# Kernel tuning notes

Hardware: AMD Instinct MI355X
Metric: run time of the kernel (lower is better)

Reference implementation:

```python
import jax, jax.numpy as jnp
import numpy as np

B, N, DK, H, A = 32, 4096, 128, 128, 128  # batch, src nodes, z dim, lstm hidden, attn dim
NEG_INF = -1e9


def setup_inputs() -> dict:
    key = jax.random.key(0)
    ks = jax.random.split(key, 12)
    sc = lambda *s: 1.0 / np.sqrt(s[-1])
    return {
        "z": jax.random.normal(ks[0], (B, N, DK), jnp.float32),
        "mask": jnp.ones((B, N), jnp.float32),
        "h0": jax.random.normal(ks[1], (B, H), jnp.float32),
        "c0": jax.random.normal(ks[2], (B, H), jnp.float32),
        # generate_lstm params (input=DK context vec, hidden=H), torch gate order i,f,g,o
        "W_ih": jax.random.normal(ks[3], (4 * H, DK), jnp.float32) * sc(DK),
        "W_hh": jax.random.normal(ks[4], (4 * H, H), jnp.float32) * sc(H),
        "b_ih": jnp.zeros((4 * H,), jnp.float32),
        "b_hh": jnp.zeros((4 * H,), jnp.float32),
        # coverage-attention params (Bahdanau + coverage, See et al. 2017)
        "W_x": jax.random.normal(ks[5], (2 * H, A), jnp.float32) * sc(2 * H),
        "W_z": jax.random.normal(ks[6], (DK, A), jnp.float32) * sc(DK),
        "w_c": jax.random.normal(ks[7], (A,), jnp.float32) * 0.1,
        "b_attn": jnp.zeros((A,), jnp.float32),
        "v": jax.random.normal(ks[8], (A,), jnp.float32) * sc(A),
        "n_node": 64,
    }


def reference(z, mask, h0, c0, W_ih, W_hh, b_ih, b_hh, W_x, W_z, w_c, b_attn, v, n_node):
    z_fea = jnp.einsum("bnd,da->bna", z, W_z)  # precomputed encoder features [B,N,A]
    mask_bool = mask > 0

    def step(carry, _):
        h, c, s, coverage, closs = carry
        # LSTM cell, torch gate order (i, f, g, o)
        gates = s @ W_ih.T + b_ih + h @ W_hh.T + b_hh  # [B,4H]
        i_g, f_g, g_g, o_g = jnp.split(gates, 4, axis=-1)
        c_new = jax.nn.sigmoid(f_g) * c + jax.nn.sigmoid(i_g) * jnp.tanh(g_g)
        h_new = jax.nn.sigmoid(o_g) * jnp.tanh(c_new)
        x = jnp.concatenate([h_new, c_new], axis=-1)  # [B,2H]
        # coverage attention
        dec_fea = x @ W_x  # [B,A]
        feat = jnp.tanh(z_fea + dec_fea[:, None, :] + coverage[..., None] * w_c + b_attn)
        e = jnp.einsum("bna,a->bn", feat, v)  # [B,N]
        e = jnp.where(mask_bool, e, NEG_INF)
        attn = jax.nn.softmax(e, axis=-1)  # [B,N]
        c_t = jnp.einsum("bn,bnd->bd", attn, z)  # context [B,DK]
        closs = closs + jnp.mean(jnp.sum(jnp.minimum(attn, coverage), axis=1))
        s_new = jax.lax.stop_gradient(c_t)  # torch: s = c_t.data
        coverage_new = coverage + attn
        return (h_new, c_new, s_new, coverage_new, closs), (c_t, attn)

    init = (h0, c0, jnp.zeros((B, DK), z.dtype), jnp.zeros((B, N), z.dtype), jnp.asarray(0.0, z.dtype))
    (_, _, _, _, closs), (cts, attns) = jax.lax.scan(step, init, None, length=n_node)
    text = jnp.transpose(cts, (1, 0, 2))        # [B, n_node, DK]
    attentions = jnp.transpose(attns, (1, 0, 2))  # [B, n_node, N]
    return text, attentions, closs
```

## Files before the change

### kernel.cpp

```cpp
#include <hip/hip_runtime.h>
#include <hip/hip_bf16.h>
#include <hip/hip_fp16.h>
#include <math.h>

#define B 32
#define NN 4096
#define DK 128
#define HH 128
#define AA 128
#define NCH 32
#define CHN 128

static const size_t OFF_ZF   = 0;
static const size_t OFF_ZH   = OFF_ZF + (size_t)B*NN*AA/2;
static const size_t OFF_P    = OFF_ZH + (size_t)B*NN*DK/2;
static const size_t OFF_COV  = OFF_P + (size_t)B*NN;
static const size_t OFF_SRED = OFF_COV + (size_t)B*NN;
static const size_t OFF_PCTX = OFF_SRED + 2*B;
static const size_t OFF_PSUM = OFF_PCTX + (size_t)B*NCH*DK;
static const size_t OFF_PCL  = OFF_PSUM + (size_t)B*NCH;
static const size_t OFF_DECQ = OFF_PCL + (size_t)B*NCH;
static const size_t OFF_HST  = OFF_DECQ + (size_t)B*AA;
static const size_t OFF_CST  = OFF_HST + (size_t)B*HH;
static const size_t OFF_CLA  = OFF_CST + (size_t)B*HH;

__device__ __forceinline__ float fast_tanh(float x) {
    float e = __expf(2.f * x);
    return 1.f - 2.f / (e + 1.f);
}
__device__ __forceinline__ float fast_sig(float x) {
    return 1.f / (1.f + __expf(-x));
}

__device__ void lstm_phase(int tid, int b, const float* __restrict__ sm_s,
                           float* hst, float* cst, float* decq,
                           const float* __restrict__ W_ih, const float* __restrict__ W_hh,
                           const float* __restrict__ b_ih, const float* __restrict__ b_hh,
                           const float* __restrict__ W_x, const float* __restrict__ b_attn)
{
    __shared__ float sm_h[HH];
    __shared__ float sm_g[4 * HH];
    __shared__ float sm_x[2 * HH];
    if (tid < HH) sm_h[tid] = hst[b * HH + tid];
    __syncthreads();
    if (tid < 256) {
        int j0 = tid, j1 = tid + 256;
        float g0 = b_ih[j0] + b_hh[j0];
        float g1 = b_ih[j1] + b_hh[j1];
        const float4* wi0 = (const float4*)(W_ih + (size_t)j0 * DK);
        const float4* wh0 = (const float4*)(W_hh + (size_t)j0 * HH);
        const float4* wi1 = (const float4*)(W_ih + (size_t)j1 * DK);
        const float4* wh1 = (const float4*)(W_hh + (size_t)j1 * HH);
        #pragma unroll 8
        for (int d4 = 0; d4 < DK / 4; ++d4) {
            float4 s4 = ((const float4*)sm_s)[d4];
            float4 h4 = ((const float4*)sm_h)[d4];
            float4 a0 = wi0[d4], a1 = wi1[d4];
            float4 c0 = wh0[d4], c1 = wh1[d4];
            g0 += s4.x*a0.x + s4.y*a0.y + s4.z*a0.z + s4.w*a0.w
                + h4.x*c0.x + h4.y*c0.y + h4.z*c0.z + h4.w*c0.w;
            g1 += s4.x*a1.x + s4.y*a1.y + s4.z*a1.z + s4.w*a1.w
                + h4.x*c1.x + h4.y*c1.y + h4.z*c1.z + h4.w*c1.w;
        }
        sm_g[j0] = g0; sm_g[j1] = g1;
    }
    __syncthreads();
    if (tid < HH) {
        float ig = sm_g[tid], fg = sm_g[HH + tid];
        float gg = sm_g[2 * HH + tid], og = sm_g[3 * HH + tid];
        float cold = cst[b * HH + tid];
        float cn = fast_sig(fg) * cold + fast_sig(ig) * fast_tanh(gg);
        float hn = fast_sig(og) * fast_tanh(cn);
        cst[b * HH + tid] = cn;
        hst[b * HH + tid] = hn;
        sm_x[tid] = hn;
        sm_x[HH + tid] = cn;
    }
    __syncthreads();
    if (tid < AA) {
        float df = b_attn[tid];
        #pragma unroll 8
        for (int k4 = 0; k4 < (2 * HH) / 4; ++k4) {
            float4 xv = ((const float4*)sm_x)[k4];
            df += xv.x * W_x[(size_t)(4 * k4 + 0) * AA + tid]
                + xv.y * W_x[(size_t)(4 * k4 + 1) * AA + tid]
                + xv.z * W_x[(size_t)(4 * k4 + 2) * AA + tid]
                + xv.w * W_x[(size_t)(4 * k4 + 3) * AA + tid];
        }
        decq[b * AA + tid] = df;
    }
    __syncthreads();
}

__global__ __launch_bounds__(256) void zfea_kernel(const float* __restrict__ z,
                                                   const float* __restrict__ Wz,
                                                   __half* __restrict__ zfh,
                                                   __half* __restrict__ zh)
{
    __shared__ float sz[32 * DK];
    const int tid = threadIdx.x;
    const size_t r0 = (size_t)blockIdx.x * 32;
    const float4* zsrc = (const float4*)(z + r0 * DK);
    float4* sz4 = (float4*)sz;
    #pragma unroll
    for (int i = 0; i < 4; ++i) sz4[i * 256 + tid] = zsrc[i * 256 + tid];
    __syncthreads();

    {
        __half2* zh2o = (__half2*)zh;
        #pragma unroll
        for (int k = 0; k < (32 * DK / 2) / 256; ++k) {
            int i = k * 256 + tid;
            __half2 hz = __floats2half2_rn(sz[2 * i], sz[2 * i + 1]);
            zh2o[r0 * (DK / 2) + i] = hz;
        }
    }

    const int a4 = tid & 31;
    const int g  = tid >> 5;
    float4 acc[4];
    #pragma unroll
    for (int r = 0; r < 4; ++r) acc[r] = make_float4(0.f, 0.f, 0.f, 0.f);
    const float4* Wz4 = (const float4*)Wz;
    for (int d4 = 0; d4 < 32; ++d4) {
        float4 w0 = Wz4[(4 * d4 + 0) * 32 + a4];
        float4 w1 = Wz4[(4 * d4 + 1) * 32 + a4];
        float4 w2 = Wz4[(4 * d4 + 2) * 32 + a4];
        float4 w3 = Wz4[(4 * d4 + 3) * 32 + a4];
        #pragma unroll
        for (int r = 0; r < 4; ++r) {
            float4 zv = *(const float4*)(&sz[(g * 4 + r) * DK + 4 * d4]);
            acc[r].x += zv.x * w0.x + zv.y * w1.x + zv.z * w2.x + zv.w * w3.x;
            acc[r].y += zv.x * w0.y + zv.y * w1.y + zv.z * w2.y + zv.w * w3.y;
            acc[r].z += zv.x * w0.z + zv.y * w1.z + zv.z * w2.z + zv.w * w3.z;
            acc[r].w += zv.x * w0.w + zv.y * w1.w + zv.z * w2.w + zv.w * w3.w;
        }
    }
    #pragma unroll
    for (int r = 0; r < 4; ++r) {
        __half2 h0 = __floats2half2_rn(acc[r].x, acc[r].y);
        __half2 h1 = __floats2half2_rn(acc[r].z, acc[r].w);
        __half2* dst = (__half2*)(zfh + (r0 + g * 4 + r) * AA + 4 * a4);
        dst[0] = h0;
        dst[1] = h1;
    }
}

__global__ __launch_bounds__(256) void prologue_kernel(
    const float* __restrict__ h0, const float* __restrict__ c0,
    float* cov, float* decq, float* hst, float* cst,
    float* cla, float* out_closs,
    const float* __restrict__ W_ih, const float* __restrict__ W_hh,
    const float* __restrict__ b_ih, const float* __restrict__ b_hh,
    const float* __restrict__ W_x, const float* __restrict__ b_attn)
{
    int b = blockIdx.x;
    int tid = threadIdx.x;
    float4 zero4 = make_float4(0.f, 0.f, 0.f, 0.f);
    float4* c4 = (float4*)(cov + (size_t)b * NN);
    for (int i = tid; i < NN / 4; i += 256) c4[i] = zero4;
    if (tid == 0) {
        cla[b] = 0.f;
        if (b == 0) *out_closs = 0.f;
    }
    if (tid < HH) {
        hst[b * HH + tid] = h0[b * HH + tid];
        cst[b * HH + tid] = c0[b * HH + tid];
    }
    __shared__ float sm_s[DK];
    if (tid < DK) sm_s[tid] = 0.f;
    __syncthreads();
    lstm_phase(tid, b, sm_s, hst, cst, decq, W_ih, W_hh, b_ih, b_hh, W_x, b_attn);
}

__global__ __launch_bounds__(512, 8) void attn_kernel(
    const __half* __restrict__ zh, const float* __restrict__ mask,
    const float* __restrict__ w_c, const float* __restrict__ v,
    const __half* __restrict__ zfh, float* __restrict__ p, float* __restrict__ cov,
    const float* __restrict__ Sred, float* __restrict__ pctx,
    float* __restrict__ psum, float* __restrict__ pcl,
    const float* __restrict__ decq,
    float* __restrict__ out_attn,
    int t, int T)
{
    const int tid = threadIdx.x;
    const int b = blockIdx.x & (B - 1);
    const int chunk = blockIdx.x >> 5;
    const int n0 = chunk * CHN;
    const int prv = (t ^ 1) & 1;

    __shared__ float sm_cov[CHN];
    __shared__ float sm_mask[CHN];
    __shared__ float sm_p[CHN];
    __shared__ float sm_ctx[8][DK];
    __shared__ float sm_sump[8];
    __shared__ float sm_red[2];

    if (tid < CHN) {
        int n = n0 + tid;
        size_t bn = (size_t)b * NN + n;
        float covn = cov[bn];
        float closs_part = 0.f;
        if (t > 0) {
            float invS = 1.f / Sred[prv * B + b];
            float ap = p[bn] * invS;
            __builtin_nontemporal_store(ap, &out_attn[((size_t)b * T + (t - 1)) * NN + n]);
            closs_part = fminf(ap, covn);
            covn += ap;
            cov[bn] = covn;
        }
        sm_cov[tid] = covn;
        #pragma unroll
        for (int off = 32; off; off >>= 1) closs_part += __shfl_xor(closs_part, off, 64);
        if ((tid & 63) == 0) sm_red[tid >> 6] = closs_part;
    } else if (tid < 2 * CHN) {
        sm_mask[tid - CHN] = mask[(size_t)b * NN + n0 + (tid - CHN)];
    }
    __syncthreads();

    const int w = tid >> 6, l = tid & 63;
    const int g2 = l >> 5, lane32 = l & 31;
    const float4 q4  = *(const float4*)(decq + b * AA + 4 * lane32);
    const float4 wc4 = *(const float4*)(w_c + 4 * lane32);
    const float4 v4  = *(const float4*)(v + 4 * lane32);

    float2 raw[8];
    {
        const char* zbase = (const char*)(zfh + ((size_t)b * NN + n0) * AA) + 8 * lane32;
        const int nbase = w * 16 + g2;
        #pragma unroll
        for (int it = 0; it < 8; ++it)
            raw[it] = *(const float2*)(zbase + (size_t)(nbase + 2 * it) * (AA * 2));
    }
    float sump = 0.f;
    float el[8];
    #pragma unroll
    for (int it = 0; it < 8; ++it) {
        const int nl = w * 16 + 2 * it + g2;
        const float cvn = sm_cov[nl];
        __half2 ha = *(__half2*)&raw[it].x;
        __half2 hb = *(__half2*)&raw[it].y;
        float2 fa = __half22float2(ha);
        float2 fb = __half22float2(hb);
        float x0 = fmaf(cvn, wc4.x, fa.x + q4.x);
        float x1 = fmaf(cvn, wc4.y, fa.y + q4.y);
        float x2 = fmaf(cvn, wc4.z, fb.x + q4.z);
        float x3 = fmaf(cvn, wc4.w, fb.y + q4.w);
        el[it] = fast_tanh(x0) * v4.x + fast_tanh(x1) * v4.y
               + fast_tanh(x2) * v4.z + fast_tanh(x3) * v4.w;
    }
    #pragma unroll
    for (int off = 16; off; off >>= 1) {
        #pragma unroll
        for (int it = 0; it < 8; ++it) el[it] += __shfl_xor(el[it], off, 64);
    }
    #pragma unroll
    for (int it = 0; it < 8; ++it) {
        const int nl = w * 16 + 2 * it + g2;
        float pe = (sm_mask[nl] > 0.f) ? __expf(el[it]) : 0.f;
        if (lane32 == 0) sm_p[nl] = pe;
        sump += pe;
    }
    sump += __shfl_xor(sump, 32, 64);
    if (l == 0) sm_sump[w] = sump;
    __syncthreads();

    const uint2* zh2 = (const uint2*)(zh + ((size_t)b * NN + n0) * DK);
    float4 acc = make_float4(0.f, 0.f, 0.f, 0.f);
    #pragma unroll
    for (int it = 0; it < 8; ++it) {
        const int nl = w * 16 + 2 * it + g2;
        uint2 u = zh2[(size_t)nl * 32 + lane32];
        __half2 ha = *(__half2*)&u.x;
        __half2 hb = *(__half2*)&u.y;
        float2 fa = __half22float2(ha);
        float2 fb = __half22float2(hb);
        float pe = sm_p[nl];
        acc.x = fmaf(pe, fa.x, acc.x);
        acc.y = fmaf(pe, fa.y, acc.y);
        acc.z = fmaf(pe, fb.x, acc.z);
        acc.w = fmaf(pe, fb.y, acc.w);
    }
    acc.x += __shfl_xor(acc.x, 32, 64);
    acc.y += __shfl_xor(acc.y, 32, 64);
    acc.z += __shfl_xor(acc.z, 32, 64);
    acc.w += __shfl_xor(acc.w, 32, 64);
    if (g2 == 0) *(float4*)(&sm_ctx[w][4 * lane32]) = acc;
    __syncthreads();

    if (tid < CHN) p[(size_t)b * NN + n0 + tid] = sm_p[tid];
    if (tid < DK) {
        float r = 0.f;
        #pragma unroll
        for (int ww = 0; ww < 8; ++ww) r += sm_ctx[ww][tid];
        pctx[((size_t)b * NCH + chunk) * DK + tid] = r;
    } else if (tid == DK) {
        float s8 = 0.f;
        #pragma unroll
        for (int ww = 0; ww < 8; ++ww) s8 += sm_sump[ww];
        psum[b * NCH + chunk] = s8;
    } else if (tid == DK + 1) {
        pcl[b * NCH + chunk] = sm_red[0] + sm_red[1];
    }
}

__global__ __launch_bounds__(256) void finish_kernel(
    const float* __restrict__ pctx, const float* __restrict__ psum,
    const float* __restrict__ pcl,
    float* __restrict__ Sred, float* __restrict__ cla,
    float* __restrict__ out_text,
    float* hst, float* cst, float* decq,
    const float* __restrict__ W_ih, const float* __restrict__ W_hh,
    const float* __restrict__ b_ih, const float* __restrict__ b_hh,
    const float* __restrict__ W_x, const float* __restrict__ b_attn,
    int t, int T)
{
    const int b = blockIdx.x;
    const int tid = threadIdx.x;
    const int cur = t & 1;
    __shared__ float sm_s[DK];
    __shared__ float sm_S;

    float r = 0.f;
    if (tid < DK) {
        #pragma unroll
        for (int k = 0; k < NCH; ++k)
            r += pctx[((size_t)b * NCH + k) * DK + tid];
    } else if (tid == DK) {
        float s = 0.f;
        #pragma unroll
        for (int k = 0; k < NCH; ++k) s += psum[b * NCH + k];
        sm_S = s;
        Sred[cur * B + b] = s;
    } else if (tid == DK + 1) {
        float clv = 0.f;
        #pragma unroll
        for (int k = 0; k < NCH; ++k) clv += pcl[b * NCH + k];
        cla[b] += clv;
    }
    __syncthreads();
    if (tid < DK) {
        float ct = r / sm_S;
        __builtin_nontemporal_store(ct, &out_text[((size_t)b * T + t) * DK + tid]);
        sm_s[tid] = ct;
    }
    __syncthreads();
    lstm_phase(tid, b, sm_s, hst, cst, decq, W_ih, W_hh, b_ih, b_hh, W_x, b_attn);
}

__global__ __launch_bounds__(256) void epilogue_kernel(
    const float* __restrict__ p, const float* __restrict__ cov, const float* __restrict__ Sred,
    const float* __restrict__ cla,
    float* __restrict__ out_attn, float* out_closs, int T)
{
    const int tid = threadIdx.x;
    const int b = blockIdx.x & (B - 1);
    const int chunk = blockIdx.x >> 5;
    const int n = chunk * 256 + tid;
    const size_t bn = (size_t)b * NN + n;
    float invS = 1.f / Sred[((T - 1) & 1) * B + b];
    float ap = p[bn] * invS;
    __builtin_nontemporal_store(ap, &out_attn[((size_t)b * T + (T - 1)) * NN + n]);
    float cl = fminf(ap, cov[bn]);
    #pragma unroll
    for (int off = 32; off; off >>= 1) cl += __shfl_xor(cl, off, 64);
    __shared__ float sred[4];
    if ((tid & 63) == 0) sred[tid >> 6] = cl;
    __syncthreads();
    if (tid == 0) {
        float blocksum = (sred[0] + sred[1] + sred[2] + sred[3]);
        if (chunk == 0) blocksum += cla[b];
        atomicAdd(out_closs, blocksum * (1.f / B));
    }
}

extern "C" void kernel_launch(void* const* d_in, const int* in_sizes, int n_in,
                              void* d_out, int out_size, void* d_ws, size_t ws_size,
                              hipStream_t stream) {
    const float* z      = (const float*)d_in[0];
    const float* mask   = (const float*)d_in[1];
    const float* h0     = (const float*)d_in[2];
    const float* c0     = (const float*)d_in[3];
    const float* W_ih   = (const float*)d_in[4];
    const float* W_hh   = (const float*)d_in[5];
    const float* b_ih   = (const float*)d_in[6];
    const float* b_hh   = (const float*)d_in[7];
    const float* W_x    = (const float*)d_in[8];
    const float* W_z    = (const float*)d_in[9];
    const float* w_c    = (const float*)d_in[10];
    const float* b_attn = (const float*)d_in[11];
    const float* v      = (const float*)d_in[12];

    int T = (out_size - 1) / (B * (NN + DK));
    if (T < 1) T = 1;

    float* ws   = (float*)d_ws;
    __half* zfh = (__half*)(ws + OFF_ZF);
    __half* zh  = (__half*)(ws + OFF_ZH);
    float* p    = ws + OFF_P;
    float* cov  = ws + OFF_COV;
    float* Sr   = ws + OFF_SRED;
    float* pctx = ws + OFF_PCTX;
    float* psum = ws + OFF_PSUM;
    float* pcl  = ws + OFF_PCL;
    float* decq = ws + OFF_DECQ;
    float* hst  = ws + OFF_HST;
    float* cst  = ws + OFF_CST;
    float* cla  = ws + OFF_CLA;

    float* out_text  = (float*)d_out;
    float* out_attn  = out_text + (size_t)B * T * DK;
    float* out_closs = out_attn + (size_t)B * T * NN;

    zfea_kernel<<<(B * NN) / 32, 256, 0, stream>>>(z, W_z, zfh, zh);
    prologue_kernel<<<B, 256, 0, stream>>>(h0, c0, cov, decq, hst, cst,
                                           cla, out_closs,
                                           W_ih, W_hh, b_ih, b_hh, W_x, b_attn);
    for (int t = 0; t < T; ++t) {
        attn_kernel<<<B * NCH, 512, 0, stream>>>(zh, mask, w_c, v, zfh, p, cov,
                                                 Sr, pctx, psum, pcl, decq,
                                                 out_attn, t, T);
        finish_kernel<<<B, 256, 0, stream>>>(pctx, psum, pcl, Sr, cla, out_text,
                                             hst, cst, decq,
                                             W_ih, W_hh, b_ih, b_hh, W_x, b_attn,
                                             t, T);
    }
    epilogue_kernel<<<512, 256, 0, stream>>>(p, cov, Sr, cla, out_attn, out_closs, T);
}
```

Baseline: 2.780 ms.

## Widen attn loads to 16B, keep exp weights in registers, drop barrier

Each wavefront now maps 16 lanes per node row and loads 16-byte chunks of the fp16 encoder features and z, instead of 32 lanes with 8-byte loads. The softmax weights stay in registers for the context accumulation, which removes a __syncthreads and the shared-memory read of the weights. The z loads can now be issued before the weighted sum. The launch-bounds occupancy hint is relaxed to give the compiler more registers, at the cost of possibly fewer resident waves and more shuffle steps per reduction.

```diff
diff --git a/kernel.cpp b/kernel.cpp
--- a/kernel.cpp
+++ b/kernel.cpp
@@ -173,7 +173,7 @@
     lstm_phase(tid, b, sm_s, hst, cst, decq, W_ih, W_hh, b_ih, b_hh, W_x, b_attn);
 }
 
-__global__ __launch_bounds__(512, 8) void attn_kernel(
+__global__ __launch_bounds__(512) void attn_kernel(
     const __half* __restrict__ zh, const float* __restrict__ mask,
     const float* __restrict__ w_c, const float* __restrict__ v,
     const __half* __restrict__ zfh, float* __restrict__ p, float* __restrict__ cov,
@@ -219,73 +219,103 @@
     __syncthreads();
 
     const int w = tid >> 6, l = tid & 63;
-    const int g2 = l >> 5, lane32 = l & 31;
-    const float4 q4  = *(const float4*)(decq + b * AA + 4 * lane32);
-    const float4 wc4 = *(const float4*)(w_c + 4 * lane32);
-    const float4 v4  = *(const float4*)(v + 4 * lane32);
-
-    float2 raw[8];
+    const int g = l >> 4, k = l & 15;
+    const float4 qa  = *(const float4*)(decq + b * AA + 8 * k);
+    const float4 qb  = *(const float4*)(decq + b * AA + 8 * k + 4);
+    const float4 wca = *(const float4*)(w_c + 8 * k);
+    const float4 wcb = *(const float4*)(w_c + 8 * k + 4);
+    const float4 va  = *(const float4*)(v + 8 * k);
+    const float4 vb  = *(const float4*)(v + 8 * k + 4);
+
+    uint4 raw[4];
     {
-        const char* zbase = (const char*)(zfh + ((size_t)b * NN + n0) * AA) + 8 * lane32;
-        const int nbase = w * 16 + g2;
-        #pragma unroll
-        for (int it = 0; it < 8; ++it)
-            raw[it] = *(const float2*)(zbase + (size_t)(nbase + 2 * it) * (AA * 2));
-    }
+        const char* zfbase = (const char*)(zfh + ((size_t)b * NN + n0) * AA) + 16 * k;
+        #pragma unroll
+        for (int it = 0; it < 4; ++it) {
+            const int nl = w * 16 + 4 * it + g;
+            raw[it] = *(const uint4*)(zfbase + (size_t)nl * 256);
+        }
+    }
+    float el[4];
+    #pragma unroll
+    for (int it = 0; it < 4; ++it) {
+        const int nl = w * 16 + 4 * it + g;
+        const float cvn = sm_cov[nl];
+        const __half2* h = (const __half2*)&raw[it];
+        float2 f0 = __half22float2(h[0]);
+        float2 f1 = __half22float2(h[1]);
+        float2 f2 = __half22float2(h[2]);
+        float2 f3 = __half22float2(h[3]);
+        el[it] = fast_tanh(fmaf(cvn, wca.x, f0.x + qa.x)) * va.x
+               + fast_tanh(fmaf(cvn, wca.y, f0.y + qa.y)) * va.y
+               + fast_tanh(fmaf(cvn, wca.z, f1.x + qa.z)) * va.z
+               + fast_tanh(fmaf(cvn, wca.w, f1.y + qa.w)) * va.w
+               + fast_tanh(fmaf(cvn, wcb.x, f2.x + qb.x)) * vb.x
+               + fast_tanh(fmaf(cvn, wcb.y, f2.y + qb.y)) * vb.y
+               + fast_tanh(fmaf(cvn, wcb.z, f3.x + qb.z)) * vb.z
+               + fast_tanh(fmaf(cvn, wcb.w, f3.y + qb.w)) * vb.w;
+    }
+    #pragma unroll
+    for (int off = 1; off <= 8; off <<= 1) {
+        #pragma unroll
+        for (int it = 0; it < 4; ++it) el[it] += __shfl_xor(el[it], off, 64);
+    }
+    float pe[4];
     float sump = 0.f;
-    float el[8];
-    #pragma unroll
-    for (int it = 0; it < 8; ++it) {
-        const int nl = w * 16 + 2 * it + g2;
-        const float cvn = sm_cov[nl];
-        __half2 ha = *(__half2*)&raw[it].x;
-        __half2 hb = *(__half2*)&raw[it].y;
-        float2 fa = __half22float2(ha);
-        float2 fb = __half22float2(hb);
-        float x0 = fmaf(cvn, wc4.x, fa.x + q4.x);
-        float x1 = fmaf(cvn, wc4.y, fa.y + q4.y);
-        float x2 = fmaf(cvn, wc4.z, fb.x + q4.z);
-        float x3 = fmaf(cvn, wc4.w, fb.y + q4.w);
-        el[it] = fast_tanh(x0) * v4.x + fast_tanh(x1) * v4.y
-               + fast_tanh(x2) * v4.z + fast_tanh(x3) * v4.w;
-    }
-    #pragma unroll
-    for (int off = 16; off; off >>= 1) {
-        #pragma unroll
-        for (int it = 0; it < 8; ++it) el[it] += __shfl_xor(el[it], off, 64);
-    }
-    #pragma unroll
-    for (int it = 0; it < 8; ++it) {
-        const int nl = w * 16 + 2 * it + g2;
-        float pe = (sm_mask[nl] > 0.f) ? __expf(el[it]) : 0.f;
-        if (lane32 == 0) sm_p[nl] = pe;
-        sump += pe;
-    }
+    #pragma unroll
+    for (int it = 0; it < 4; ++it) {
+        const int nl = w * 16 + 4 * it + g;
+        pe[it] = (sm_mask[nl] > 0.f) ? __expf(el[it]) : 0.f;
+        if (k == 0) sm_p[nl] = pe[it];
+        sump += pe[it];
+    }
+    sump += __shfl_xor(sump, 16, 64);
     sump += __shfl_xor(sump, 32, 64);
     if (l == 0) sm_sump[w] = sump;
-    __syncthreads();
-
-    const uint2* zh2 = (const uint2*)(zh + ((size_t)b * NN + n0) * DK);
-    float4 acc = make_float4(0.f, 0.f, 0.f, 0.f);
-    #pragma unroll
-    for (int it = 0; it < 8; ++it) {
-        const int nl = w * 16 + 2 * it + g2;
-        uint2 u = zh2[(size_t)nl * 32 + lane32];
-        __half2 ha = *(__half2*)&u.x;
-        __half2 hb = *(__half2*)&u.y;
-        float2 fa = __half22float2(ha);
-        float2 fb = __half22float2(hb);
-        float pe = sm_p[nl];
-        acc.x = fmaf(pe, fa.x, acc.x);
-        acc.y = fmaf(pe, fa.y, acc.y);
-        acc.z = fmaf(pe, fb.x, acc.z);
-        acc.w = fmaf(pe, fb.y, acc.w);
-    }
-    acc.x += __shfl_xor(acc.x, 32, 64);
-    acc.y += __shfl_xor(acc.y, 32, 64);
-    acc.z += __shfl_xor(acc.z, 32, 64);
-    acc.w += __shfl_xor(acc.w, 32, 64);
-    if (g2 == 0) *(float4*)(&sm_ctx[w][4 * lane32]) = acc;
+
+    uint4 rz[4];
+    {
+        const char* zhbase = (const char*)(zh + ((size_t)b * NN + n0) * DK) + 16 * k;
+        #pragma unroll
+        for (int it = 0; it < 4; ++it) {
+            const int nl = w * 16 + 4 * it + g;
+            rz[it] = *(const uint4*)(zhbase + (size_t)nl * 256);
+        }
+    }
+    float4 acA = make_float4(0.f, 0.f, 0.f, 0.f);
+    float4 acB = make_float4(0.f, 0.f, 0.f, 0.f);
+    #pragma unroll
+    for (int it = 0; it < 4; ++it) {
+        const __half2* h = (const __half2*)&rz[it];
+        float2 f0 = __half22float2(h[0]);
+        float2 f1 = __half22float2(h[1]);
+        float2 f2 = __half22float2(h[2]);
+        float2 f3 = __half22float2(h[3]);
+        const float pv = pe[it];
+        acA.x = fmaf(pv, f0.x, acA.x);
+        acA.y = fmaf(pv, f0.y, acA.y);
+        acA.z = fmaf(pv, f1.x, acA.z);
+        acA.w = fmaf(pv, f1.y, acA.w);
+        acB.x = fmaf(pv, f2.x, acB.x);
+        acB.y = fmaf(pv, f2.y, acB.y);
+        acB.z = fmaf(pv, f3.x, acB.z);
+        acB.w = fmaf(pv, f3.y, acB.w);
+    }
+    #pragma unroll
+    for (int off = 16; off <= 32; off <<= 1) {
+        acA.x += __shfl_xor(acA.x, off, 64);
+        acA.y += __shfl_xor(acA.y, off, 64);
+        acA.z += __shfl_xor(acA.z, off, 64);
+        acA.w += __shfl_xor(acA.w, off, 64);
+        acB.x += __shfl_xor(acB.x, off, 64);
+        acB.y += __shfl_xor(acB.y, off, 64);
+        acB.z += __shfl_xor(acB.z, off, 64);
+        acB.w += __shfl_xor(acB.w, off, 64);
+    }
+    if (g == 0) {
+        *(float4*)(&sm_ctx[w][8 * k])     = acA;
+        *(float4*)(&sm_ctx[w][8 * k + 4]) = acB;
+    }
     __syncthreads();
 
     if (tid < CHN) p[(size_t)b * NN + n0 + tid] = sm_p[tid];
```

Measured after the change: 2.780 ms. Within noise of the previous version (+0.0%).
